# Performance work log

Hardware: AMD Instinct MI355X
Metric: run time of the kernel (lower is better)

Reference implementation:

```python
import jax, jax.numpy as jnp
import numpy as np

K = 8  # search_range in sample_wise_recolor
BIG = 1e30


def setup_inputs() -> dict:
    key = jax.random.key(0)
    ks = jax.random.split(key, 6)
    L, N = 16384, 10000  # L: upsampled candidate voxels (multiple of 8), N: target points
    pred_F = jax.random.normal(ks[0], (L,), jnp.float32)
    cand_xyz = jax.random.normal(ks[1], (L, 3), jnp.float32) * 50.0
    cand_rgb = jax.random.uniform(ks[2], (L, 3), jnp.float32)
    tgt_xyz = jax.random.normal(ks[3], (N, 3), jnp.float32) * 50.0
    tgt_rgb = jax.random.uniform(ks[4], (N, 3), jnp.float32)
    keep_target = jax.random.randint(ks[5], (L,), 0, 2, jnp.int32)
    return {"pred_F": pred_F, "cand_xyz": cand_xyz, "cand_rgb": cand_rgb,
            "tgt_xyz": tgt_xyz, "tgt_rgb": tgt_rgb, "keep_target": keep_target,
            "points_num": 8192}


def _get_keep(pred, points_num):
    # local-max mask over groups of 8 children (scatter of per-row argmax)
    L = pred.shape[0]
    p8 = pred.reshape(-1, 8)
    rows = jnp.arange(p8.shape[0])
    is_local_max = jnp.zeros(p8.shape, dtype=bool).at[rows, jnp.argmax(p8, axis=1)].set(True).reshape(-1)
    # kthvalue over the non-local-max subset: local-max entries pushed to +inf so the
    # k-th smallest of the full sorted array equals the k-th smallest of the subset.
    k = L - points_num  # static python int
    vals = jnp.where(is_local_max, jnp.inf, pred)
    threshold = jnp.sort(vals)[k - 1]
    return (pred > threshold) | is_local_max


def _pairwise_sqdist(a, b):
    # a: [P,3], b: [Q,3] -> [P,Q] squared distances
    a2 = jnp.sum(a * a, axis=1)
    b2 = jnp.sum(b * b, axis=1)
    d2 = a2[:, None] + b2[None, :] - 2.0 * (a @ b.T)
    return jnp.maximum(d2, 0.0)


def _recolor_loss(cand_xyz, rgb, keep, tgt_xyz, tgt_rgb):
    L = cand_xyz.shape[0]
    N = tgt_xyz.shape[0]
    d2 = _pairwise_sqdist(tgt_xyz, cand_xyz)  # [N, L]

    # ---- recolor_backward: KNN from each target point into kept candidates ----
    d_masked = jnp.where(keep[None, :], d2, BIG)
    neg_d, idx = jax.lax.top_k(-d_masked, K)  # [N, K]
    d = -neg_d
    zero_mask = d == 0.0
    min_mask = (d == jnp.min(d, axis=1, keepdims=True)) & ~jnp.any(zero_mask, axis=1)[:, None]
    w = jnp.where(min_mask, 1.0 / jnp.sqrt(jnp.maximum(d, 1e-30)), 0.0)  # [N, K]

    flat_idx = idx.reshape(-1)
    num = jnp.zeros((L, 3), rgb.dtype).at[flat_idx].add((tgt_rgb[:, None, :] * w[:, :, None]).reshape(-1, 3))
    den = jnp.zeros((L,), rgb.dtype).at[flat_idx].add(w.reshape(-1))
    has_den = den != 0.0
    recolored = jnp.where(has_den[:, None], num / jnp.where(has_den, den, 1.0)[:, None], 0.0)

    # exact-match (zero-distance) targets overwrite; scatter with safe out-of-range dummy row
    safe_idx = jnp.where(zero_mask, idx, L).reshape(-1)
    tgt_exp = jnp.broadcast_to(tgt_rgb[:, None, :], (N, K, 3)).reshape(-1, 3)
    recolored = jnp.concatenate([recolored, jnp.zeros((1, 3), rgb.dtype)], 0).at[safe_idx].set(tgt_exp)[:L]
    empty = jnp.concatenate([~has_den, jnp.zeros((1,), bool)], 0).at[safe_idx].set(False)[:L]
    empty = empty & keep  # only kept candidates matter

    # ---- recolor_forward: kept candidates with no color yet pull from nearest targets ----
    neg_df, idxf = jax.lax.top_k(-d2.T, K)  # [L, K]
    df = -neg_df
    mf = df == jnp.min(df, axis=1, keepdims=True)
    rec_fwd = jnp.sum(tgt_rgb[idxf] * mf[:, :, None], axis=1) / jnp.sum(mf, axis=1, keepdims=True).astype(rgb.dtype)
    recolored = jnp.where(empty[:, None], rec_fwd, recolored)

    # L1 loss over kept candidates only; recolor target is no-grad in the original
    recolored = jax.lax.stop_gradient(recolored)
    return jnp.sum(jnp.where(keep[:, None], jnp.abs(rgb - recolored), 0.0))


def reference(pred_F, cand_xyz, cand_rgb, tgt_xyz, tgt_rgb, keep_target, points_num):
    keep = _get_keep(jax.lax.stop_gradient(pred_F), points_num)  # @torch.no_grad
    # coord recon loss: BCE-with-logits, reduction='sum'
    t = keep_target.astype(pred_F.dtype)
    coord_loss = jnp.sum(jnp.maximum(pred_F, 0.0) - pred_F * t + jnp.log1p(jnp.exp(-jnp.abs(pred_F))))
    # inverse_transform_for_color in training mode: x * 255
    rgb = cand_rgb * 255.0
    rgb_loss = _recolor_loss(cand_xyz, rgb, keep, tgt_xyz, tgt_rgb)
    return jnp.stack([coord_loss, rgb_loss])
```

## Files before the change

### kernel.cpp

```cpp
#include <hip/hip_runtime.h>
#include <hip/hip_bf16.h>


typedef unsigned long long ull;

__global__ __launch_bounds__(256) void k_prep(
    const float* __restrict__ pred, const float* __restrict__ txyz,
    float4* __restrict__ ttile, float4* __restrict__ numden,
    int* __restrict__ zerohit, unsigned int* __restrict__ key,
    unsigned char* __restrict__ islm, int* __restrict__ counters,
    float* __restrict__ out, int L, int N) {
  int gidx = blockIdx.x * 256 + threadIdx.x;
  int gsz = (int)gridDim.x * 256;
  for (int i = gidx; i < N; i += gsz) {
    float x = txyz[3*i], y = txyz[3*i+1], z = txyz[3*i+2];
    ttile[i] = make_float4(x, y, z, fmaf(x, x, fmaf(y, y, z * z)));
  }
  for (int i = gidx; i < L; i += gsz) {
    numden[i] = make_float4(0.f, 0.f, 0.f, 0.f);
    zerohit[i] = 0;
  }
  if (gidx < 8) counters[gidx] = 0;
  if (gidx < 2) out[gidx] = 0.f;
  int ngroups = L >> 3;
  for (int g = gidx; g < ngroups; g += gsz) {
    const float4* pv = (const float4*)pred + (size_t)g * 2;
    float4 a = pv[0], b = pv[1];
    float v[8] = {a.x, a.y, a.z, a.w, b.x, b.y, b.z, b.w};
    int bi = 0; float bv = v[0];
    #pragma unroll
    for (int j = 1; j < 8; ++j) if (v[j] > bv) { bv = v[j]; bi = j; }
    unsigned int kk[8];
    ull lmpack = 0ull;
    #pragma unroll
    for (int j = 0; j < 8; ++j) {
      unsigned int fb = __float_as_uint(v[j]);
      unsigned int mk = (fb & 0x80000000u) ? ~fb : (fb | 0x80000000u);
      if (j == bi) { mk = 0xFF800000u; lmpack |= 1ull << (8 * j); }
      kk[j] = mk;
    }
    ((uint4*)key)[g*2]   = make_uint4(kk[0], kk[1], kk[2], kk[3]);
    ((uint4*)key)[g*2+1] = make_uint4(kk[4], kk[5], kk[6], kk[7]);
    *(ull*)(islm + (size_t)g * 8) = lmpack;
  }
}

__device__ __forceinline__ void select_bin(
    unsigned int* hist, int nb, unsigned int rank,
    unsigned int* sB, unsigned int* sR, int tid) {
  if (tid < 64) {
    int g = nb >> 6;
    unsigned int sum = 0;
    for (int j = 0; j < g; ++j) sum += hist[tid * g + j];
    unsigned int incl = sum;
    for (int o = 1; o < 64; o <<= 1) {
      unsigned int v = __shfl_up(incl, o);
      if (tid >= o) incl += v;
    }
    unsigned int excl = incl - sum;
    bool cond = (rank >= excl) && (rank < incl);
    unsigned long long bal = __ballot(cond);
    int first = __ffsll((long long)bal) - 1;
    if (tid == first) {
      unsigned int r = rank - excl, cum = 0;
      for (int j = 0; j < g; ++j) {
        unsigned int c = hist[tid * g + j];
        if (r < cum + c) { *sB = (unsigned int)(tid * g + j); *sR = r - cum; break; }
        cum += c;
      }
    }
  }
}

__global__ __launch_bounds__(256) void k_sel(
    const unsigned int* __restrict__ key, const int* __restrict__ pnum_p,
    float* __restrict__ thr_out, int L) {
  __shared__ unsigned int hist[2048];
  __shared__ unsigned int sB, sR;
  int tid = threadIdx.x;
  unsigned int rank = (unsigned int)(L - pnum_p[0] - 1);
  const uint4* k4 = (const uint4*)key;
  int n4 = L >> 2;
  for (int b = tid; b < 2048; b += 256) hist[b] = 0u;
  __syncthreads();
  for (int i = tid; i < n4; i += 256) {
    uint4 v = k4[i];
    atomicAdd(&hist[v.x >> 21], 1u); atomicAdd(&hist[v.y >> 21], 1u);
    atomicAdd(&hist[v.z >> 21], 1u); atomicAdd(&hist[v.w >> 21], 1u);
  }
  __syncthreads();
  select_bin(hist, 2048, rank, &sB, &sR, tid);
  __syncthreads();
  unsigned int B1 = sB, R1 = sR;
  for (int b = tid; b < 2048; b += 256) hist[b] = 0u;
  __syncthreads();
  for (int i = tid; i < n4; i += 256) {
    uint4 v = k4[i];
    if ((v.x >> 21) == B1) atomicAdd(&hist[(v.x >> 10) & 2047u], 1u);
    if ((v.y >> 21) == B1) atomicAdd(&hist[(v.y >> 10) & 2047u], 1u);
    if ((v.z >> 21) == B1) atomicAdd(&hist[(v.z >> 10) & 2047u], 1u);
    if ((v.w >> 21) == B1) atomicAdd(&hist[(v.w >> 10) & 2047u], 1u);
  }
  __syncthreads();
  select_bin(hist, 2048, R1, &sB, &sR, tid);
  __syncthreads();
  unsigned int B2 = sB, R2 = sR;
  for (int b = tid; b < 1024; b += 256) hist[b] = 0u;
  __syncthreads();
  unsigned int top22 = (B1 << 11) | B2;
  for (int i = tid; i < n4; i += 256) {
    uint4 v = k4[i];
    if ((v.x >> 10) == top22) atomicAdd(&hist[v.x & 1023u], 1u);
    if ((v.y >> 10) == top22) atomicAdd(&hist[v.y & 1023u], 1u);
    if ((v.z >> 10) == top22) atomicAdd(&hist[v.z & 1023u], 1u);
    if ((v.w >> 10) == top22) atomicAdd(&hist[v.w & 1023u], 1u);
  }
  __syncthreads();
  select_bin(hist, 1024, R2, &sB, &sR, tid);
  __syncthreads();
  if (tid == 0) {
    unsigned int fkey = (B1 << 21) | (B2 << 10) | sB;
    unsigned int fb = (fkey & 0x80000000u) ? (fkey & 0x7FFFFFFFu) : ~fkey;
    thr_out[0] = __uint_as_float(fb);
  }
}

__global__ __launch_bounds__(256) void k_keepc(
    const float* __restrict__ pred, const unsigned char* __restrict__ islm,
    const float* __restrict__ thr_p, const float* __restrict__ cxyz,
    const int* __restrict__ ktgt, int* __restrict__ keep,
    float4* __restrict__ klist, int* __restrict__ kidx,
    int* __restrict__ counters, float* __restrict__ out, int L) {
  int i = blockIdx.x * 256 + threadIdx.x;
  float thr = thr_p[0];
  float term = 0.f;
  if (i < L) {
    float p = pred[i];
    bool kp = (p > thr) || islm[i];
    keep[i] = kp ? 1 : 0;
    if (kp) {
      int pos = atomicAdd(&counters[0], 1);
      float x = cxyz[3*i], y = cxyz[3*i+1], z = cxyz[3*i+2];
      klist[pos] = make_float4(x, y, z, fmaf(x, x, fmaf(y, y, z * z)));
      kidx[pos] = i;
    }
    float t = (float)ktgt[i];
    term = fmaxf(p, 0.f) - p * t + log1pf(expf(-fabsf(p)));
  }
  for (int o = 32; o > 0; o >>= 1) term += __shfl_down(term, o);
  if ((threadIdx.x & 63) == 0) atomicAdd(&out[0], term);
}

__global__ __launch_bounds__(256) void k_scanw(
    const float* __restrict__ txyz, const float4* __restrict__ klist,
    const int* __restrict__ kidx, const float4* __restrict__ ttile,
    const int* __restrict__ counters, ull* __restrict__ tmin,
    int* __restrict__ fidx, int L, int N, int NBW) {
  int tid = threadIdx.x;
  int lane = tid & 63;
  int wv = tid >> 6;
  int kc = counters[0];
  int bid = blockIdx.x;

  const float4* list; int listn; int q0;
  float qx[8], qy[8], qz[8];
  if (bid < NBW) {
    q0 = (bid * 4 + wv) * 8;
    #pragma unroll
    for (int j = 0; j < 8; ++j) {
      int a = min(q0 + j, N - 1);
      qx[j] = txyz[3*a]; qy[j] = txyz[3*a+1]; qz[j] = txyz[3*a+2];
    }
    list = klist; listn = kc;
  } else {
    int eb = (bid - NBW) * 32;
    if (eb >= kc) return;
    q0 = eb + wv * 8;
    #pragma unroll
    for (int j = 0; j < 8; ++j) {
      int a = min(q0 + j, kc - 1);
      float4 A = klist[a];
      qx[j] = A.x; qy[j] = A.y; qz[j] = A.z;
    }
    list = ttile; listn = N;
  }
  float nx[8], ny[8], nz[8], bb[8]; int ii[8];
  #pragma unroll
  for (int j = 0; j < 8; ++j) {
    nx[j] = -2.f * qx[j]; ny[j] = -2.f * qy[j]; nz[j] = -2.f * qz[j];
    bb[j] = 3e38f; ii[j] = 0;
  }

  int i = lane;
  for (; i + 64 < listn; i += 128) {
    float4 A = list[i];
    float4 B = list[i + 64];
    #pragma unroll
    for (int j = 0; j < 8; ++j) {
      float dA = fmaf(nx[j], A.x, A.w);
      dA = fmaf(ny[j], A.y, dA);
      dA = fmaf(nz[j], A.z, dA);
      if (dA < bb[j]) { bb[j] = dA; ii[j] = i; }
      float dB = fmaf(nx[j], B.x, B.w);
      dB = fmaf(ny[j], B.y, dB);
      dB = fmaf(nz[j], B.z, dB);
      if (dB < bb[j]) { bb[j] = dB; ii[j] = i + 64; }
    }
  }
  if (i < listn) {
    float4 A = list[i];
    #pragma unroll
    for (int j = 0; j < 8; ++j) {
      float dA = fmaf(nx[j], A.x, A.w);
      dA = fmaf(ny[j], A.y, dA);
      dA = fmaf(nz[j], A.z, dA);
      if (dA < bb[j]) { bb[j] = dA; ii[j] = i; }
    }
  }

  #pragma unroll
  for (int o = 32; o > 0; o >>= 1) {
    #pragma unroll
    for (int j = 0; j < 8; ++j) {
      float ob = __shfl_xor(bb[j], o);
      int   oi = __shfl_xor(ii[j], o);
      if (ob < bb[j] || (ob == bb[j] && oi < ii[j])) { bb[j] = ob; ii[j] = oi; }
    }
  }
  if (lane == 0) {
    if (bid < NBW) {
      #pragma unroll
      for (int j = 0; j < 8; ++j) {
        int t = q0 + j;
        if (t < N) {
          float4 cd = klist[ii[j]];
          float dx = txyz[3*t] - cd.x, dy = txyz[3*t+1] - cd.y, dz = txyz[3*t+2] - cd.z;
          float dtrue = fmaf(dx, dx, fmaf(dy, dy, dz * dz));
          tmin[t] = ((ull)__float_as_uint(dtrue) << 32) | (unsigned int)kidx[ii[j]];
        }
      }
    } else {
      #pragma unroll
      for (int j = 0; j < 8; ++j) {
        int e = q0 + j;
        if (e < kc) fidx[kidx[e]] = ii[j];
      }
    }
  }
}

__global__ __launch_bounds__(256) void k_scatter(
    const float* __restrict__ trgb, const ull* __restrict__ tmin,
    float4* __restrict__ numden, int* __restrict__ zerohit,
    float4* __restrict__ zcolor, int N) {
  int t = blockIdx.x * 256 + threadIdx.x;
  if (t >= N) return;
  ull pack = tmin[t];
  float d = __uint_as_float((unsigned int)(pack >> 32));
  int idx = (int)(pack & 0xFFFFFFFFull);
  float r = trgb[3*t], g = trgb[3*t+1], b = trgb[3*t+2];
  if (d == 0.0f) {
    zerohit[idx] = 1;
    zcolor[idx] = make_float4(r, g, b, 0.f);
  } else {
    float w = 1.0f / sqrtf(fmaxf(d, 1e-30f));
    atomicAdd(&numden[idx].x, r * w);
    atomicAdd(&numden[idx].y, g * w);
    atomicAdd(&numden[idx].z, b * w);
    atomicAdd(&numden[idx].w, w);
  }
}

__global__ __launch_bounds__(256) void k_loss(
    const float* __restrict__ crgb, const float* __restrict__ trgb,
    const int* __restrict__ keep, const float4* __restrict__ numden,
    const int* __restrict__ zerohit, const float4* __restrict__ zcolor,
    const int* __restrict__ fidx, float* __restrict__ out, int L) {
  int l = blockIdx.x * 256 + threadIdx.x;
  float loss = 0.f;
  if (l < L && keep[l]) {
    float rr, rg, rb;
    if (zerohit[l]) {
      float4 z = zcolor[l]; rr = z.x; rg = z.y; rb = z.z;
    } else {
      float4 nd = numden[l];
      if (nd.w != 0.f) { rr = nd.x / nd.w; rg = nd.y / nd.w; rb = nd.z / nd.w; }
      else {
        int ti = fidx[l];
        rr = trgb[3*ti]; rg = trgb[3*ti+1]; rb = trgb[3*ti+2];
      }
    }
    float sr = crgb[3*l]*255.f, sg = crgb[3*l+1]*255.f, sb = crgb[3*l+2]*255.f;
    loss = fabsf(sr - rr) + fabsf(sg - rg) + fabsf(sb - rb);
  }
  for (int o = 32; o > 0; o >>= 1) loss += __shfl_down(loss, o);
  if ((threadIdx.x & 63) == 0) atomicAdd(&out[1], loss);
}

extern "C" void kernel_launch(void* const* d_in, const int* in_sizes, int n_in,
                              void* d_out, int out_size, void* d_ws, size_t ws_size,
                              hipStream_t stream) {
  const float* pred = (const float*)d_in[0];
  const float* cxyz = (const float*)d_in[1];
  const float* crgb = (const float*)d_in[2];
  const float* txyz = (const float*)d_in[3];
  const float* trgb = (const float*)d_in[4];
  const int*   ktgt = (const int*)d_in[5];
  const int*   pnum = (const int*)d_in[6];
  int L = in_sizes[0];
  int N = in_sizes[3] / 3;

  char* ws = (char*)d_ws;
  size_t off = 0;
  float4* klist  = (float4*)(ws + off);   off += (size_t)L * 16;
  float4* ttile  = (float4*)(ws + off);   off += (size_t)((N + 3) & ~3) * 16;
  float4* numden = (float4*)(ws + off);   off += (size_t)L * 16;
  float4* zcolor = (float4*)(ws + off);   off += (size_t)L * 16;
  unsigned int* key = (unsigned int*)(ws + off); off += (size_t)L * 4;
  ull* tmin      = (ull*)(ws + off);      off += (size_t)((N + 1) & ~1) * 8;
  int* keep      = (int*)(ws + off);      off += (size_t)L * 4;
  int* kidx      = (int*)(ws + off);      off += (size_t)L * 4;
  int* zerohit   = (int*)(ws + off);      off += (size_t)L * 4;
  int* fidx      = (int*)(ws + off);      off += (size_t)L * 4;
  float* thr_slot = (float*)(ws + off);   off += 16;
  int* counters  = (int*)(ws + off);      off += 256;
  unsigned char* islm = (unsigned char*)(ws + off); off += ((size_t)L + 15) & ~15ull;
  float* out = (float*)d_out;

  int nbL = (L + 255) / 256;
  int nbN = (N + 255) / 256;
  int NBW = (N + 31) / 32;
  int NFW = (L + 31) / 32;
  int mx = max(L, N);

  k_prep<<<(mx + 255) / 256, 256, 0, stream>>>(
      pred, txyz, ttile, numden, zerohit, key, islm, counters, out, L, N);

  k_sel<<<1, 256, 0, stream>>>(key, pnum, thr_slot, L);

  k_keepc<<<nbL, 256, 0, stream>>>(
      pred, islm, thr_slot, cxyz, ktgt, keep, klist, kidx, counters, out, L);

  k_scanw<<<NBW + NFW, 256, 0, stream>>>(
      txyz, klist, kidx, ttile, counters, tmin, fidx, L, N, NBW);

  k_scatter<<<nbN, 256, 0, stream>>>(trgb, tmin, numden, zerohit, zcolor, N);

  k_loss<<<nbL, 256, 0, stream>>>(
      crgb, trgb, keep, numden, zerohit, zcolor, fidx, out, L);
}
```

Measured before the change: 147.7 us.

## Replace brute-force nearest-neighbour scans with uniform-grid spatial search

Swaps the all-pairs nearest-neighbour scans (targets into kept candidates, and kept candidates into targets) for a 16^3 uniform grid. A bounding-box reduction sets up the grid, per-cell histograms and a prefix scan build cell offsets, and a counting sort buckets both point sets. Each query then searches outward shell by shell and stops once no unvisited cell can be closer than the current best. This removes the quadratic distance work but adds two small kernels, atomics, and divergent per-thread search loops whose cost depends on how the points are distributed.

```diff
diff --git a/kernel.cpp b/kernel.cpp
--- a/kernel.cpp
+++ b/kernel.cpp
@@ -3,23 +3,94 @@
 
 
 typedef unsigned long long ull;
+#define GR 16
+
+__device__ __forceinline__ int cell_clamp(float v, float b0, float ih) {
+  int c = (int)((v - b0) * ih);
+  return min(max(c, 0), GR - 1);
+}
+__device__ __forceinline__ int cell_of(float x, float y, float z,
+                                       const float* gp) {
+  int cx = cell_clamp(x, gp[0], gp[6]);
+  int cy = cell_clamp(y, gp[1], gp[7]);
+  int cz = cell_clamp(z, gp[2], gp[8]);
+  return (cz * GR + cy) * GR + cx;
+}
+
+__device__ void nn_search(
+    float qx, float qy, float qz,
+    const int* __restrict__ start, const float4* __restrict__ pts,
+    const float* gp, float* obest, int* oidx) {
+  float bx0 = gp[0], by0 = gp[1], bz0 = gp[2];
+  float hx = gp[3], hy = gp[4], hz = gp[5];
+  int cx = cell_clamp(qx, bx0, gp[6]);
+  int cy = cell_clamp(qy, by0, gp[7]);
+  int cz = cell_clamp(qz, bz0, gp[8]);
+  float best = 3e38f; int bi = 0;
+  for (int R = 0; R <= GR; ++R) {
+    int zlo = max(cz - R, 0), zhi = min(cz + R, GR - 1);
+    int ylo = max(cy - R, 0), yhi = min(cy + R, GR - 1);
+    int xlo = max(cx - R, 0), xhi = min(cx + R, GR - 1);
+    for (int zz = zlo; zz <= zhi; ++zz) {
+      int adz = (zz > cz) ? zz - cz : cz - zz;
+      for (int yy = ylo; yy <= yhi; ++yy) {
+        int ady = (yy > cy) ? yy - cy : cy - yy;
+        bool face = (adz == R) || (ady == R);
+        for (int xx = xlo; xx <= xhi; ++xx) {
+          int adx = (xx > cx) ? xx - cx : cx - xx;
+          if (!face && adx != R) continue;
+          int cid = (zz * GR + yy) * GR + xx;
+          int s = start[cid], e = start[cid + 1];
+          for (int p = s; p < e; ++p) {
+            float4 P = pts[p];
+            float dx = qx - P.x, dy = qy - P.y, dz = qz - P.z;
+            float d = fmaf(dx, dx, fmaf(dy, dy, dz * dz));
+            if (d < best) { best = d; bi = __float_as_int(P.w); }
+          }
+        }
+      }
+    }
+    float dmin = 3e38f;
+    if (cx - R > 0)      dmin = fminf(dmin, qx - (bx0 + (cx - R) * hx));
+    if (cx + R < GR - 1) dmin = fminf(dmin, (bx0 + (cx + R + 1) * hx) - qx);
+    if (cy - R > 0)      dmin = fminf(dmin, qy - (by0 + (cy - R) * hy));
+    if (cy + R < GR - 1) dmin = fminf(dmin, (by0 + (cy + R + 1) * hy) - qy);
+    if (cz - R > 0)      dmin = fminf(dmin, qz - (bz0 + (cz - R) * hz));
+    if (cz + R < GR - 1) dmin = fminf(dmin, (bz0 + (cz + R + 1) * hz) - qz);
+    if (dmin == 3e38f) break;
+    float dm = fmaxf(dmin, 0.f);
+    if (dm * dm >= best) break;
+  }
+  *obest = best; *oidx = bi;
+}
 
 __global__ __launch_bounds__(256) void k_prep(
     const float* __restrict__ pred, const float* __restrict__ txyz,
-    float4* __restrict__ ttile, float4* __restrict__ numden,
+    const float* __restrict__ cxyz, float4* __restrict__ numden,
     int* __restrict__ zerohit, unsigned int* __restrict__ key,
-    unsigned char* __restrict__ islm, int* __restrict__ counters,
+    unsigned char* __restrict__ islm, unsigned int* __restrict__ chist,
+    unsigned int* __restrict__ thist, float4* __restrict__ blockmin,
+    float4* __restrict__ blockmax, int* __restrict__ counters,
     float* __restrict__ out, int L, int N) {
-  int gidx = blockIdx.x * 256 + threadIdx.x;
+  __shared__ float bmn[4][3], bmx[4][3];
+  int tid = threadIdx.x, lane = tid & 63, wv = tid >> 6;
+  int gidx = blockIdx.x * 256 + tid;
   int gsz = (int)gridDim.x * 256;
+  float mnx = 3e38f, mny = 3e38f, mnz = 3e38f;
+  float mxx = -3e38f, mxy = -3e38f, mxz = -3e38f;
   for (int i = gidx; i < N; i += gsz) {
     float x = txyz[3*i], y = txyz[3*i+1], z = txyz[3*i+2];
-    ttile[i] = make_float4(x, y, z, fmaf(x, x, fmaf(y, y, z * z)));
+    mnx = fminf(mnx, x); mny = fminf(mny, y); mnz = fminf(mnz, z);
+    mxx = fmaxf(mxx, x); mxy = fmaxf(mxy, y); mxz = fmaxf(mxz, z);
   }
   for (int i = gidx; i < L; i += gsz) {
+    float x = cxyz[3*i], y = cxyz[3*i+1], z = cxyz[3*i+2];
+    mnx = fminf(mnx, x); mny = fminf(mny, y); mnz = fminf(mnz, z);
+    mxx = fmaxf(mxx, x); mxy = fmaxf(mxy, y); mxz = fmaxf(mxz, z);
     numden[i] = make_float4(0.f, 0.f, 0.f, 0.f);
     zerohit[i] = 0;
   }
+  for (int i = gidx; i < GR*GR*GR; i += gsz) { chist[i] = 0u; thist[i] = 0u; }
   if (gidx < 8) counters[gidx] = 0;
   if (gidx < 2) out[gidx] = 0.f;
   int ngroups = L >> 3;
@@ -43,6 +114,29 @@
     ((uint4*)key)[g*2+1] = make_uint4(kk[4], kk[5], kk[6], kk[7]);
     *(ull*)(islm + (size_t)g * 8) = lmpack;
   }
+  #pragma unroll
+  for (int o = 32; o > 0; o >>= 1) {
+    mnx = fminf(mnx, __shfl_xor(mnx, o)); mny = fminf(mny, __shfl_xor(mny, o));
+    mnz = fminf(mnz, __shfl_xor(mnz, o)); mxx = fmaxf(mxx, __shfl_xor(mxx, o));
+    mxy = fmaxf(mxy, __shfl_xor(mxy, o)); mxz = fmaxf(mxz, __shfl_xor(mxz, o));
+  }
+  if (lane == 0) {
+    bmn[wv][0] = mnx; bmn[wv][1] = mny; bmn[wv][2] = mnz;
+    bmx[wv][0] = mxx; bmx[wv][1] = mxy; bmx[wv][2] = mxz;
+  }
+  __syncthreads();
+  if (tid == 0) {
+    for (int w = 1; w < 4; ++w) {
+      bmn[0][0] = fminf(bmn[0][0], bmn[w][0]);
+      bmn[0][1] = fminf(bmn[0][1], bmn[w][1]);
+      bmn[0][2] = fminf(bmn[0][2], bmn[w][2]);
+      bmx[0][0] = fmaxf(bmx[0][0], bmx[w][0]);
+      bmx[0][1] = fmaxf(bmx[0][1], bmx[w][1]);
+      bmx[0][2] = fmaxf(bmx[0][2], bmx[w][2]);
+    }
+    blockmin[blockIdx.x] = make_float4(bmn[0][0], bmn[0][1], bmn[0][2], 0.f);
+    blockmax[blockIdx.x] = make_float4(bmx[0][0], bmx[0][1], bmx[0][2], 0.f);
+  }
 }
 
 __device__ __forceinline__ void select_bin(
@@ -74,7 +168,8 @@
 
 __global__ __launch_bounds__(256) void k_sel(
     const unsigned int* __restrict__ key, const int* __restrict__ pnum_p,
-    float* __restrict__ thr_out, int L) {
+    const float4* __restrict__ blockmin, const float4* __restrict__ blockmax,
+    float* __restrict__ thr_out, float* __restrict__ gparams, int L, int nbp) {
   __shared__ unsigned int hist[2048];
   __shared__ unsigned int sB, sR;
   int tid = threadIdx.x;
@@ -123,14 +218,39 @@
     unsigned int fb = (fkey & 0x80000000u) ? (fkey & 0x7FFFFFFFu) : ~fkey;
     thr_out[0] = __uint_as_float(fb);
   }
+  if (tid < 64) {
+    float mnx = 3e38f, mny = 3e38f, mnz = 3e38f;
+    float mxx = -3e38f, mxy = -3e38f, mxz = -3e38f;
+    if (tid < nbp) {
+      float4 mn = blockmin[tid], mx = blockmax[tid];
+      mnx = mn.x; mny = mn.y; mnz = mn.z;
+      mxx = mx.x; mxy = mx.y; mxz = mx.z;
+    }
+    #pragma unroll
+    for (int o = 32; o > 0; o >>= 1) {
+      mnx = fminf(mnx, __shfl_xor(mnx, o)); mny = fminf(mny, __shfl_xor(mny, o));
+      mnz = fminf(mnz, __shfl_xor(mnz, o)); mxx = fmaxf(mxx, __shfl_xor(mxx, o));
+      mxy = fmaxf(mxy, __shfl_xor(mxy, o)); mxz = fmaxf(mxz, __shfl_xor(mxz, o));
+    }
+    if (tid == 0) {
+      float sx = fmaxf(mxx - mnx, 1e-9f);
+      float sy = fmaxf(mxy - mny, 1e-9f);
+      float sz = fmaxf(mxz - mnz, 1e-9f);
+      gparams[0] = mnx; gparams[1] = mny; gparams[2] = mnz;
+      gparams[3] = sx / GR; gparams[4] = sy / GR; gparams[5] = sz / GR;
+      gparams[6] = GR / sx; gparams[7] = GR / sy; gparams[8] = GR / sz;
+    }
+  }
 }
 
 __global__ __launch_bounds__(256) void k_keepc(
     const float* __restrict__ pred, const unsigned char* __restrict__ islm,
     const float* __restrict__ thr_p, const float* __restrict__ cxyz,
-    const int* __restrict__ ktgt, int* __restrict__ keep,
+    const float* __restrict__ txyz, const int* __restrict__ ktgt,
+    const float* __restrict__ gparams, int* __restrict__ keep,
     float4* __restrict__ klist, int* __restrict__ kidx,
-    int* __restrict__ counters, float* __restrict__ out, int L) {
+    unsigned int* __restrict__ chist, unsigned int* __restrict__ thist,
+    int* __restrict__ counters, float* __restrict__ out, int L, int N) {
   int i = blockIdx.x * 256 + threadIdx.x;
   float thr = thr_p[0];
   float term = 0.f;
@@ -141,110 +261,103 @@
     if (kp) {
       int pos = atomicAdd(&counters[0], 1);
       float x = cxyz[3*i], y = cxyz[3*i+1], z = cxyz[3*i+2];
-      klist[pos] = make_float4(x, y, z, fmaf(x, x, fmaf(y, y, z * z)));
+      klist[pos] = make_float4(x, y, z, 0.f);
       kidx[pos] = i;
+      atomicAdd(&chist[cell_of(x, y, z, gparams)], 1u);
     }
     float t = (float)ktgt[i];
     term = fmaxf(p, 0.f) - p * t + log1pf(expf(-fabsf(p)));
   }
+  if (i < N) {
+    atomicAdd(&thist[cell_of(txyz[3*i], txyz[3*i+1], txyz[3*i+2], gparams)], 1u);
+  }
   for (int o = 32; o > 0; o >>= 1) term += __shfl_down(term, o);
   if ((threadIdx.x & 63) == 0) atomicAdd(&out[0], term);
 }
 
-__global__ __launch_bounds__(256) void k_scanw(
-    const float* __restrict__ txyz, const float4* __restrict__ klist,
-    const int* __restrict__ kidx, const float4* __restrict__ ttile,
-    const int* __restrict__ counters, ull* __restrict__ tmin,
-    int* __restrict__ fidx, int L, int N, int NBW) {
-  int tid = threadIdx.x;
-  int lane = tid & 63;
-  int wv = tid >> 6;
+__global__ __launch_bounds__(256) void k_pfx(
+    const unsigned int* __restrict__ chist, const unsigned int* __restrict__ thist,
+    int* __restrict__ cstart, int* __restrict__ tstart,
+    int* __restrict__ ccur, int* __restrict__ tcur) {
+  __shared__ unsigned int wsum[4];
+  int tid = threadIdx.x, lane = tid & 63, wv = tid >> 6;
+  const int NC = GR * GR * GR;
+  const int PER = NC / 256;
+  for (int h = 0; h < 2; ++h) {
+    const unsigned int* hist = h ? thist : chist;
+    int* st = h ? tstart : cstart;
+    int* cur = h ? tcur : ccur;
+    unsigned int loc[PER];
+    unsigned int s = 0;
+    int base = tid * PER;
+    #pragma unroll
+    for (int j = 0; j < PER; ++j) { loc[j] = s; s += hist[base + j]; }
+    unsigned int incl = s;
+    for (int o = 1; o < 64; o <<= 1) {
+      unsigned int v = __shfl_up(incl, o);
+      if (lane >= o) incl += v;
+    }
+    if (lane == 63) wsum[wv] = incl;
+    __syncthreads();
+    unsigned int woff = 0;
+    for (int w = 0; w < wv; ++w) woff += wsum[w];
+    unsigned int excl = woff + incl - s;
+    #pragma unroll
+    for (int j = 0; j < PER; ++j) {
+      int v = (int)(excl + loc[j]);
+      st[base + j] = v; cur[base + j] = v;
+    }
+    if (tid == 255) st[NC] = (int)(excl + s);
+    __syncthreads();
+  }
+}
+
+__global__ __launch_bounds__(256) void k_sort(
+    const float4* __restrict__ klist, const int* __restrict__ kidx,
+    const int* __restrict__ counters, const float* __restrict__ txyz,
+    const float* __restrict__ gparams, int* __restrict__ ccur,
+    int* __restrict__ tcur, float4* __restrict__ csorted,
+    float4* __restrict__ tsorted, int N) {
   int kc = counters[0];
-  int bid = blockIdx.x;
-
-  const float4* list; int listn; int q0;
-  float qx[8], qy[8], qz[8];
-  if (bid < NBW) {
-    q0 = (bid * 4 + wv) * 8;
-    #pragma unroll
-    for (int j = 0; j < 8; ++j) {
-      int a = min(q0 + j, N - 1);
-      qx[j] = txyz[3*a]; qy[j] = txyz[3*a+1]; qz[j] = txyz[3*a+2];
-    }
-    list = klist; listn = kc;
+  int gidx = blockIdx.x * 256 + threadIdx.x;
+  int gsz = (int)gridDim.x * 256;
+  for (int i = gidx; i < kc; i += gsz) {
+    float4 cd = klist[i];
+    int cid = cell_of(cd.x, cd.y, cd.z, gparams);
+    int pos = atomicAdd(&ccur[cid], 1);
+    csorted[pos] = make_float4(cd.x, cd.y, cd.z, __int_as_float(kidx[i]));
+  }
+  for (int i = gidx; i < N; i += gsz) {
+    float x = txyz[3*i], y = txyz[3*i+1], z = txyz[3*i+2];
+    int cid = cell_of(x, y, z, gparams);
+    int pos = atomicAdd(&tcur[cid], 1);
+    tsorted[pos] = make_float4(x, y, z, __int_as_float(i));
+  }
+}
+
+__global__ __launch_bounds__(256) void k_nn(
+    const float4* __restrict__ csorted, const int* __restrict__ cstart,
+    const float4* __restrict__ tsorted, const int* __restrict__ tstart,
+    const int* __restrict__ counters, const float* __restrict__ gparams,
+    ull* __restrict__ tmin, int* __restrict__ fidx, int L, int N) {
+  int q = blockIdx.x * 256 + threadIdx.x;
+  int kc = counters[0];
+  float gp[9];
+  #pragma unroll
+  for (int j = 0; j < 9; ++j) gp[j] = gparams[j];
+  if (q < N) {
+    float4 Q = tsorted[q];
+    float best; int bi;
+    nn_search(Q.x, Q.y, Q.z, cstart, csorted, gp, &best, &bi);
+    int t = __float_as_int(Q.w);
+    tmin[t] = ((ull)__float_as_uint(best) << 32) | (unsigned int)bi;
   } else {
-    int eb = (bid - NBW) * 32;
-    if (eb >= kc) return;
-    q0 = eb + wv * 8;
-    #pragma unroll
-    for (int j = 0; j < 8; ++j) {
-      int a = min(q0 + j, kc - 1);
-      float4 A = klist[a];
-      qx[j] = A.x; qy[j] = A.y; qz[j] = A.z;
-    }
-    list = ttile; listn = N;
-  }
-  float nx[8], ny[8], nz[8], bb[8]; int ii[8];
-  #pragma unroll
-  for (int j = 0; j < 8; ++j) {
-    nx[j] = -2.f * qx[j]; ny[j] = -2.f * qy[j]; nz[j] = -2.f * qz[j];
-    bb[j] = 3e38f; ii[j] = 0;
-  }
-
-  int i = lane;
-  for (; i + 64 < listn; i += 128) {
-    float4 A = list[i];
-    float4 B = list[i + 64];
-    #pragma unroll
-    for (int j = 0; j < 8; ++j) {
-      float dA = fmaf(nx[j], A.x, A.w);
-      dA = fmaf(ny[j], A.y, dA);
-      dA = fmaf(nz[j], A.z, dA);
-      if (dA < bb[j]) { bb[j] = dA; ii[j] = i; }
-      float dB = fmaf(nx[j], B.x, B.w);
-      dB = fmaf(ny[j], B.y, dB);
-      dB = fmaf(nz[j], B.z, dB);
-      if (dB < bb[j]) { bb[j] = dB; ii[j] = i + 64; }
-    }
-  }
-  if (i < listn) {
-    float4 A = list[i];
-    #pragma unroll
-    for (int j = 0; j < 8; ++j) {
-      float dA = fmaf(nx[j], A.x, A.w);
-      dA = fmaf(ny[j], A.y, dA);
-      dA = fmaf(nz[j], A.z, dA);
-      if (dA < bb[j]) { bb[j] = dA; ii[j] = i; }
-    }
-  }
-
-  #pragma unroll
-  for (int o = 32; o > 0; o >>= 1) {
-    #pragma unroll
-    for (int j = 0; j < 8; ++j) {
-      float ob = __shfl_xor(bb[j], o);
-      int   oi = __shfl_xor(ii[j], o);
-      if (ob < bb[j] || (ob == bb[j] && oi < ii[j])) { bb[j] = ob; ii[j] = oi; }
-    }
-  }
-  if (lane == 0) {
-    if (bid < NBW) {
-      #pragma unroll
-      for (int j = 0; j < 8; ++j) {
-        int t = q0 + j;
-        if (t < N) {
-          float4 cd = klist[ii[j]];
-          float dx = txyz[3*t] - cd.x, dy = txyz[3*t+1] - cd.y, dz = txyz[3*t+2] - cd.z;
-          float dtrue = fmaf(dx, dx, fmaf(dy, dy, dz * dz));
-          tmin[t] = ((ull)__float_as_uint(dtrue) << 32) | (unsigned int)kidx[ii[j]];
-        }
-      }
-    } else {
-      #pragma unroll
-      for (int j = 0; j < 8; ++j) {
-        int e = q0 + j;
-        if (e < kc) fidx[kidx[e]] = ii[j];
-      }
+    int f = q - N;
+    if (f < kc) {
+      float4 Q = csorted[f];
+      float best; int bi;
+      nn_search(Q.x, Q.y, Q.z, tstart, tsorted, gp, &best, &bi);
+      fidx[__float_as_int(Q.w)] = bi;
     }
   }
 }
@@ -309,40 +422,58 @@
   const int*   pnum = (const int*)d_in[6];
   int L = in_sizes[0];
   int N = in_sizes[3] / 3;
+  const int NC = GR * GR * GR;
 
   char* ws = (char*)d_ws;
   size_t off = 0;
-  float4* klist  = (float4*)(ws + off);   off += (size_t)L * 16;
-  float4* ttile  = (float4*)(ws + off);   off += (size_t)((N + 3) & ~3) * 16;
-  float4* numden = (float4*)(ws + off);   off += (size_t)L * 16;
-  float4* zcolor = (float4*)(ws + off);   off += (size_t)L * 16;
+  float4* klist   = (float4*)(ws + off);  off += (size_t)L * 16;
+  float4* csorted = (float4*)(ws + off);  off += (size_t)L * 16;
+  float4* tsorted = (float4*)(ws + off);  off += (size_t)((N + 3) & ~3) * 16;
+  float4* numden  = (float4*)(ws + off);  off += (size_t)L * 16;
+  float4* zcolor  = (float4*)(ws + off);  off += (size_t)L * 16;
+  float4* blockmin = (float4*)(ws + off); off += 64 * 16;
+  float4* blockmax = (float4*)(ws + off); off += 64 * 16;
   unsigned int* key = (unsigned int*)(ws + off); off += (size_t)L * 4;
-  ull* tmin      = (ull*)(ws + off);      off += (size_t)((N + 1) & ~1) * 8;
-  int* keep      = (int*)(ws + off);      off += (size_t)L * 4;
-  int* kidx      = (int*)(ws + off);      off += (size_t)L * 4;
-  int* zerohit   = (int*)(ws + off);      off += (size_t)L * 4;
-  int* fidx      = (int*)(ws + off);      off += (size_t)L * 4;
+  ull* tmin       = (ull*)(ws + off);     off += (size_t)((N + 1) & ~1) * 8;
+  int* keep       = (int*)(ws + off);     off += (size_t)L * 4;
+  int* kidx       = (int*)(ws + off);     off += (size_t)L * 4;
+  int* zerohit    = (int*)(ws + off);     off += (size_t)L * 4;
+  int* fidx       = (int*)(ws + off);     off += (size_t)L * 4;
+  unsigned int* chist = (unsigned int*)(ws + off); off += NC * 4;
+  unsigned int* thist = (unsigned int*)(ws + off); off += NC * 4;
+  int* cstart     = (int*)(ws + off);     off += (NC + 1) * 4;
+  int* tstart     = (int*)(ws + off);     off += (NC + 1) * 4;
+  int* ccur       = (int*)(ws + off);     off += NC * 4;
+  int* tcur       = (int*)(ws + off);     off += NC * 4;
+  float* gparams  = (float*)(ws + off);   off += 16 * 4;
   float* thr_slot = (float*)(ws + off);   off += 16;
-  int* counters  = (int*)(ws + off);      off += 256;
+  int* counters   = (int*)(ws + off);     off += 256;
   unsigned char* islm = (unsigned char*)(ws + off); off += ((size_t)L + 15) & ~15ull;
   float* out = (float*)d_out;
 
   int nbL = (L + 255) / 256;
   int nbN = (N + 255) / 256;
-  int NBW = (N + 31) / 32;
-  int NFW = (L + 31) / 32;
   int mx = max(L, N);
-
-  k_prep<<<(mx + 255) / 256, 256, 0, stream>>>(
-      pred, txyz, ttile, numden, zerohit, key, islm, counters, out, L, N);
-
-  k_sel<<<1, 256, 0, stream>>>(key, pnum, thr_slot, L);
+  int nbp = (mx + 255) / 256;
+
+  k_prep<<<nbp, 256, 0, stream>>>(
+      pred, txyz, cxyz, numden, zerohit, key, islm, chist, thist,
+      blockmin, blockmax, counters, out, L, N);
+
+  k_sel<<<1, 256, 0, stream>>>(
+      key, pnum, blockmin, blockmax, thr_slot, gparams, L, nbp);
 
   k_keepc<<<nbL, 256, 0, stream>>>(
-      pred, islm, thr_slot, cxyz, ktgt, keep, klist, kidx, counters, out, L);
-
-  k_scanw<<<NBW + NFW, 256, 0, stream>>>(
-      txyz, klist, kidx, ttile, counters, tmin, fidx, L, N, NBW);
+      pred, islm, thr_slot, cxyz, txyz, ktgt, gparams,
+      keep, klist, kidx, chist, thist, counters, out, L, N);
+
+  k_pfx<<<1, 256, 0, stream>>>(chist, thist, cstart, tstart, ccur, tcur);
+
+  k_sort<<<nbL, 256, 0, stream>>>(
+      klist, kidx, counters, txyz, gparams, ccur, tcur, csorted, tsorted, N);
+
+  k_nn<<<(N + L + 255) / 256, 256, 0, stream>>>(
+      csorted, cstart, tsorted, tstart, counters, gparams, tmin, fidx, L, N);
 
   k_scatter<<<nbN, 256, 0, stream>>>(trgb, tmin, numden, zerohit, zcolor, N);
 
```

Result: slower. 314.0 us (+112.6%).
